# Kernel optimization log

Measured on AMD Instinct MI355X. Metric: run time of the kernel, lower is better.

Reference implementation:

```python
import jax, jax.numpy as jnp
import numpy as np

NUM_REGIONS = 116
EPS = 1e-6
GAMMA = 1e-3


def setup_inputs() -> dict:
    key = jax.random.key(0)
    k1, k2, k3 = jax.random.split(key, 3)
    shape = (16, 3, 512, 512)
    real = jax.random.normal(k1, shape, dtype=jnp.float32)
    fake = jax.random.normal(k2, shape, dtype=jnp.float32)
    region_map = jax.random.randint(k3, shape, 0, NUM_REGIONS, dtype=jnp.int32)
    return {"real": real, "fake": fake, "region_map": region_map}


def reference(real, fake, region_map):
    # Elementwise L1 loss (reduction='none')
    whole_loss = jnp.abs(real - fake)

    flat_ids = region_map.reshape(-1)
    flat_loss = whole_loss.reshape(-1)

    # per-region sum of loss and per-region element count.
    sums = jax.ops.segment_sum(flat_loss, flat_ids, num_segments=NUM_REGIONS)
    counts = jax.ops.segment_sum(
        jnp.ones_like(flat_loss), flat_ids, num_segments=NUM_REGIONS
    )
    rloss_mean = sums / (counts + EPS)  # [116]

    # max_l1_loss buffer starts at 0 and takes running max of detached means;
    # after the first loop it equals max(0, max_r rloss_mean), with no grad.
    max_l1 = jnp.maximum(jnp.max(jax.lax.stop_gradient(rloss_mean)), 0.0)

    # Per-region weight (rloss_mean NOT detached here, so grads flow through it)
    w = 1.0 + GAMMA * (rloss_mean / (max_l1 + EPS))  # [116]

    # sum_r w_r * (whole_loss * mask_r) == whole_loss * w[region_map]
    weighted = whole_loss * w[region_map]
    return weighted.mean()
```

## Files before the change

### kernel.cpp

```cpp
#include <hip/hip_runtime.h>

#define NUM_REGIONS 116
#define EPS 1e-6f
#define GAMMA 1e-3f

#define FIX_SCALE 1048576.0f
#define FIX_INV   (1.0f / 1048576.0f)
#define CNT_SHIFT 40
#define SUM_MASK  ((1ULL << CNT_SHIFT) - 1ULL)

typedef unsigned long long u64;

__global__ __launch_bounds__(256) void region_accum_kernel(
    const float* __restrict__ real,
    const float* __restrict__ fake,
    const int*   __restrict__ rmap,
    u64* __restrict__ g_acc,
    int n, int n4)
{
    __shared__ u64 s_acc[4][NUM_REGIONS];
    const int tid = threadIdx.x;
    u64* tbl = s_acc[tid >> 6];

    for (int i = tid; i < 4 * NUM_REGIONS; i += 256)
        (&s_acc[0][0])[i] = 0ULL;
    __syncthreads();

    const float4* real4 = (const float4*)real;
    const float4* fake4 = (const float4*)fake;
    const int4*   map4  = (const int4*)rmap;

    const int stride = gridDim.x * 256;
    for (int i = blockIdx.x * 256 + tid; i < n4; i += stride) {
        float4 a = real4[i];
        float4 b = fake4[i];
        int4   m = map4[i];
        u64 vx = (1ULL << CNT_SHIFT) | (u64)(unsigned)(fabsf(a.x - b.x) * FIX_SCALE + 0.5f);
        u64 vy = (1ULL << CNT_SHIFT) | (u64)(unsigned)(fabsf(a.y - b.y) * FIX_SCALE + 0.5f);
        u64 vz = (1ULL << CNT_SHIFT) | (u64)(unsigned)(fabsf(a.z - b.z) * FIX_SCALE + 0.5f);
        u64 vw = (1ULL << CNT_SHIFT) | (u64)(unsigned)(fabsf(a.w - b.w) * FIX_SCALE + 0.5f);
        atomicAdd(&tbl[m.x], vx);
        atomicAdd(&tbl[m.y], vy);
        atomicAdd(&tbl[m.z], vz);
        atomicAdd(&tbl[m.w], vw);
    }

    const int tail_start = n4 << 2;
    if (blockIdx.x == 0 && tid < (n - tail_start)) {
        int idx = tail_start + tid;
        u64 v = (1ULL << CNT_SHIFT) |
                (u64)(unsigned)(fabsf(real[idx] - fake[idx]) * FIX_SCALE + 0.5f);
        atomicAdd(&tbl[rmap[idx]], v);
    }
    __syncthreads();

    for (int r = tid; r < NUM_REGIONS; r += 256) {
        u64 t = s_acc[0][r] + s_acc[1][r] + s_acc[2][r] + s_acc[3][r];
        if (t) atomicAdd(&g_acc[r], t);
    }
}

__global__ __launch_bounds__(64) void region_finalize_kernel(
    const u64* __restrict__ g_acc,
    float* __restrict__ out,
    float inv_n)
{
    const int lane = threadIdx.x;
    u64 tA = g_acc[lane];
    float sA = (float)(tA & SUM_MASK) * FIX_INV;
    float cA = (float)(tA >> CNT_SHIFT);
    float mA = sA / (cA + EPS);

    float sB = 0.0f, mB = 0.0f;
    if (lane + 64 < NUM_REGIONS) {
        u64 tB = g_acc[lane + 64];
        sB = (float)(tB & SUM_MASK) * FIX_INV;
        float cB = (float)(tB >> CNT_SHIFT);
        mB = sB / (cB + EPS);
    }

    float mx = fmaxf(mA, mB);
#pragma unroll
    for (int off = 32; off > 0; off >>= 1)
        mx = fmaxf(mx, __shfl_xor(mx, off));
    mx = fmaxf(mx, 0.0f);

    const float k = GAMMA / (mx + EPS);
    float part = sA * (1.0f + mA * k) + sB * (1.0f + mB * k);
#pragma unroll
    for (int off = 32; off > 0; off >>= 1)
        part += __shfl_xor(part, off);

    if (lane == 0)
        out[0] = part * inv_n;
}

extern "C" void kernel_launch(void* const* d_in, const int* in_sizes, int n_in,
                              void* d_out, int out_size, void* d_ws, size_t ws_size,
                              hipStream_t stream) {
    const float* real = (const float*)d_in[0];
    const float* fake = (const float*)d_in[1];
    const int*   rmap = (const int*)d_in[2];
    float* out = (float*)d_out;

    const int n  = in_sizes[0];
    const int n4 = n >> 2;

    u64* g_acc = (u64*)d_ws;
    hipMemsetAsync(d_ws, 0, NUM_REGIONS * sizeof(u64), stream);

    int blocks = (n4 + 255) / 256;
    if (blocks > 2048) blocks = 2048;
    if (blocks < 1) blocks = 1;

    region_accum_kernel<<<blocks, 256, 0, stream>>>(real, fake, rmap, g_acc, n, n4);
    region_finalize_kernel<<<1, 64, 0, stream>>>(g_acc, out, 1.0f / (float)n);
}
```

Before: 183.3 us.

## Use packed 32-bit shared atomics with more sub-tables and fuse finalize via last-block

Shared-memory histogram accumulation switches from 64-bit to 32-bit packed sum/count words at lower fixed-point scale, and splits into 8 sub-tables instead of 4 to cut atomic contention. Block partials are widened to 64-bit before global atomics. The finalize kernel is removed; the last block to finish, detected via a global counter, computes the weighted mean. Narrower fields reduce precision and risk sum-field overflow for large values or dense regions.

```diff
diff --git a/kernel.cpp b/kernel.cpp
--- a/kernel.cpp
+++ b/kernel.cpp
@@ -4,95 +4,118 @@
 #define EPS 1e-6f
 #define GAMMA 1e-3f
 
-#define FIX_SCALE 1048576.0f
-#define FIX_INV   (1.0f / 1048576.0f)
-#define CNT_SHIFT 40
-#define SUM_MASK  ((1ULL << CNT_SHIFT) - 1ULL)
+#define SUM_SCALE 16384.0f
+#define SUM_INV   (1.0f / 16384.0f)
+#define CNT32_SHIFT 22
+#define SUM32_MASK ((1u << CNT32_SHIFT) - 1u)
+
+#define CNT64_SHIFT 40
+#define SUM64_MASK ((1ULL << CNT64_SHIFT) - 1ULL)
+
+#define NSUB 8
 
 typedef unsigned long long u64;
+typedef unsigned int u32;
 
-__global__ __launch_bounds__(256) void region_accum_kernel(
+__global__ __launch_bounds__(256) void region_fused_kernel(
     const float* __restrict__ real,
     const float* __restrict__ fake,
     const int*   __restrict__ rmap,
     u64* __restrict__ g_acc,
-    int n, int n4)
+    u32* __restrict__ g_ctr,
+    float* __restrict__ out,
+    int n, int n4, int nblocks, float inv_n)
 {
-    __shared__ u64 s_acc[4][NUM_REGIONS];
+    __shared__ u32 s_acc[NSUB][NUM_REGIONS];
+    __shared__ float s_red[3][128];
+    __shared__ int s_last;
+
     const int tid = threadIdx.x;
-    u64* tbl = s_acc[tid >> 6];
+    u32* tbl = s_acc[((tid >> 6) << 1) | (tid & 1)];
 
-    for (int i = tid; i < 4 * NUM_REGIONS; i += 256)
-        (&s_acc[0][0])[i] = 0ULL;
+    for (int i = tid; i < NSUB * NUM_REGIONS; i += 256)
+        (&s_acc[0][0])[i] = 0u;
     __syncthreads();
 
     const float4* real4 = (const float4*)real;
     const float4* fake4 = (const float4*)fake;
     const int4*   map4  = (const int4*)rmap;
 
-    const int stride = gridDim.x * 256;
+    const int stride = nblocks * 256;
     for (int i = blockIdx.x * 256 + tid; i < n4; i += stride) {
         float4 a = real4[i];
         float4 b = fake4[i];
         int4   m = map4[i];
-        u64 vx = (1ULL << CNT_SHIFT) | (u64)(unsigned)(fabsf(a.x - b.x) * FIX_SCALE + 0.5f);
-        u64 vy = (1ULL << CNT_SHIFT) | (u64)(unsigned)(fabsf(a.y - b.y) * FIX_SCALE + 0.5f);
-        u64 vz = (1ULL << CNT_SHIFT) | (u64)(unsigned)(fabsf(a.z - b.z) * FIX_SCALE + 0.5f);
-        u64 vw = (1ULL << CNT_SHIFT) | (u64)(unsigned)(fabsf(a.w - b.w) * FIX_SCALE + 0.5f);
+        u32 vx = (1u << CNT32_SHIFT) | (u32)(fabsf(a.x - b.x) * SUM_SCALE + 0.5f);
+        u32 vy = (1u << CNT32_SHIFT) | (u32)(fabsf(a.y - b.y) * SUM_SCALE + 0.5f);
+        u32 vz = (1u << CNT32_SHIFT) | (u32)(fabsf(a.z - b.z) * SUM_SCALE + 0.5f);
+        u32 vw = (1u << CNT32_SHIFT) | (u32)(fabsf(a.w - b.w) * SUM_SCALE + 0.5f);
         atomicAdd(&tbl[m.x], vx);
         atomicAdd(&tbl[m.y], vy);
         atomicAdd(&tbl[m.z], vz);
         atomicAdd(&tbl[m.w], vw);
     }
 
-    const int tail_start = n4 << 2;
-    if (blockIdx.x == 0 && tid < (n - tail_start)) {
-        int idx = tail_start + tid;
-        u64 v = (1ULL << CNT_SHIFT) |
-                (u64)(unsigned)(fabsf(real[idx] - fake[idx]) * FIX_SCALE + 0.5f);
+    const int tail = n4 << 2;
+    if (blockIdx.x == 0 && tid < (n - tail)) {
+        int idx = tail + tid;
+        u32 v = (1u << CNT32_SHIFT) |
+                (u32)(fabsf(real[idx] - fake[idx]) * SUM_SCALE + 0.5f);
         atomicAdd(&tbl[rmap[idx]], v);
     }
     __syncthreads();
 
-    for (int r = tid; r < NUM_REGIONS; r += 256) {
-        u64 t = s_acc[0][r] + s_acc[1][r] + s_acc[2][r] + s_acc[3][r];
-        if (t) atomicAdd(&g_acc[r], t);
+    if (tid < NUM_REGIONS) {
+        u64 sum = 0, cnt = 0;
+#pragma unroll
+        for (int k = 0; k < NSUB; ++k) {
+            u32 v = s_acc[k][tid];
+            sum += (u64)(v & SUM32_MASK);
+            cnt += (u64)(v >> CNT32_SHIFT);
+        }
+        u64 packed = (cnt << CNT64_SHIFT) | sum;
+        if (packed) atomicAdd(&g_acc[tid], packed);
     }
-}
+    __threadfence();
+    __syncthreads();
 
-__global__ __launch_bounds__(64) void region_finalize_kernel(
-    const u64* __restrict__ g_acc,
-    float* __restrict__ out,
-    float inv_n)
-{
-    const int lane = threadIdx.x;
-    u64 tA = g_acc[lane];
-    float sA = (float)(tA & SUM_MASK) * FIX_INV;
-    float cA = (float)(tA >> CNT_SHIFT);
-    float mA = sA / (cA + EPS);
+    if (tid == 0) {
+        u32 prev = atomicAdd(g_ctr, 1u);
+        s_last = (prev == (u32)(nblocks - 1)) ? 1 : 0;
+    }
+    __syncthreads();
+    if (!s_last) return;
 
-    float sB = 0.0f, mB = 0.0f;
-    if (lane + 64 < NUM_REGIONS) {
-        u64 tB = g_acc[lane + 64];
-        sB = (float)(tB & SUM_MASK) * FIX_INV;
-        float cB = (float)(tB >> CNT_SHIFT);
-        mB = sB / (cB + EPS);
+    __threadfence();
+    float mean = 0.f, ssum = 0.f;
+    if (tid < NUM_REGIONS) {
+        u64 t = atomicAdd(&g_acc[tid], 0ULL);
+        ssum = (float)(t & SUM64_MASK) * SUM_INV;
+        float c = (float)(t >> CNT64_SHIFT);
+        mean = ssum / (c + EPS);
     }
-
-    float mx = fmaxf(mA, mB);
+    if (tid < 128) {
+        s_red[0][tid] = mean;
+        s_red[1][tid] = ssum;
+        s_red[2][tid] = ssum * mean;
+    }
+    __syncthreads();
+    if (tid < 64) {
+        float mx = fmaxf(s_red[0][tid], s_red[0][tid + 64]);
+        float a  = s_red[1][tid] + s_red[1][tid + 64];
+        float b  = s_red[2][tid] + s_red[2][tid + 64];
 #pragma unroll
-    for (int off = 32; off > 0; off >>= 1)
-        mx = fmaxf(mx, __shfl_xor(mx, off));
-    mx = fmaxf(mx, 0.0f);
-
-    const float k = GAMMA / (mx + EPS);
-    float part = sA * (1.0f + mA * k) + sB * (1.0f + mB * k);
-#pragma unroll
-    for (int off = 32; off > 0; off >>= 1)
-        part += __shfl_xor(part, off);
-
-    if (lane == 0)
-        out[0] = part * inv_n;
+        for (int off = 32; off > 0; off >>= 1) {
+            mx = fmaxf(mx, __shfl_xor(mx, off));
+            a += __shfl_xor(a, off);
+            b += __shfl_xor(b, off);
+        }
+        if (tid == 0) {
+            mx = fmaxf(mx, 0.0f);
+            const float k = GAMMA / (mx + EPS);
+            out[0] = (a + k * b) * inv_n;
+        }
+    }
 }
 
 extern "C" void kernel_launch(void* const* d_in, const int* in_sizes, int n_in,
@@ -107,12 +130,13 @@
     const int n4 = n >> 2;
 
     u64* g_acc = (u64*)d_ws;
-    hipMemsetAsync(d_ws, 0, NUM_REGIONS * sizeof(u64), stream);
+    u32* g_ctr = (u32*)((char*)d_ws + NUM_REGIONS * sizeof(u64));
+    hipMemsetAsync(d_ws, 0, NUM_REGIONS * sizeof(u64) + sizeof(u32), stream);
 
-    int blocks = (n4 + 255) / 256;
-    if (blocks > 2048) blocks = 2048;
-    if (blocks < 1) blocks = 1;
+    int nblocks = (n4 + 255) / 256;
+    if (nblocks > 2048) nblocks = 2048;
+    if (nblocks < 1) nblocks = 1;
 
-    region_accum_kernel<<<blocks, 256, 0, stream>>>(real, fake, rmap, g_acc, n, n4);
-    region_finalize_kernel<<<1, 64, 0, stream>>>(g_acc, out, 1.0f / (float)n);
+    region_fused_kernel<<<nblocks, 256, 0, stream>>>(
+        real, fake, rmap, g_acc, g_ctr, out, n, n4, nblocks, 1.0f / (float)n);
 }
```

Result: slower. 437.8 us (+138.9%).
